# Kernel optimization log

Hardware: AMD Instinct MI355X
Metric: run time of the kernel (lower is better)

Reference implementation:

```python
import jax, jax.numpy as jnp
import numpy as np

N_NODES = 100000
N_EDGES = 1600000
D = 128
L = 3


def setup_inputs() -> dict:
    key = jax.random.key(0)
    ks = jax.random.split(key, 5)
    x = jax.random.normal(ks[0], (N_NODES, D), dtype=jnp.float32)
    # Xavier-ish scale for stability through 3 layers
    scale = 1.0 / np.sqrt(D)
    W_self = jax.random.normal(ks[1], (L, D, D), dtype=jnp.float32) * scale
    W_neigh = jax.random.normal(ks[2], (L, D, D), dtype=jnp.float32) * scale
    bias = jnp.zeros((L, D), dtype=jnp.float32)
    src = jax.random.randint(ks[3], (N_EDGES,), 0, N_NODES)
    dst = jax.random.randint(ks[4], (N_EDGES,), 0, N_NODES)
    return {"x": x, "W_self": W_self, "W_neigh": W_neigh, "bias": bias,
            "src": src, "dst": dst}


def reference(x, W_self, W_neigh, bias, src, dst):
    """HomoSAGEEncoder forward (inference mode, dropout = identity).

    Each layer: DGL SAGEConv('mean'):
        h_neigh[v] = mean_{u in in-neighbors(v)} h[u]   (0 if no neighbors)
        h = h @ W_self + h_neigh @ W_neigh + bias
    followed by ReLU.
    """
    N = x.shape[0]
    n_layers = W_self.shape[0]
    # in-degree per destination node (shared across layers)
    deg = jax.ops.segment_sum(jnp.ones_like(dst, dtype=x.dtype), dst,
                              num_segments=N)
    inv_deg = (1.0 / jnp.maximum(deg, 1.0))[:, None]  # [N,1]

    h = x
    for l in range(n_layers):
        msg = h[src]  # [E,D] gather
        h_neigh = jax.ops.segment_sum(msg, dst, num_segments=N) * inv_deg
        h = h @ W_self[l] + h_neigh @ W_neigh[l] + bias[l]
        h = jax.nn.relu(h)
        # dropout is identity at inference; skipped
    return h
```

## Files before the change

### kernel.cpp

```cpp
#include <hip/hip_runtime.h>

typedef __attribute__((ext_vector_type(8))) short short8;
typedef __attribute__((ext_vector_type(4))) float f32x4;

static constexpr int NN = 100000;
static constexpr int NE = 1600000;
static constexpr int DD = 128;
static constexpr int SCAN_CHUNK = 1024;
static constexpr int NB = (NN + SCAN_CHUNK - 1) / SCAN_CHUNK;

static constexpr int OFF_DEG  = 0;
static constexpr int OFF_OFFS = NN;
static constexpr int OFF_CUR  = 2*NN + 2;
static constexpr int OFF_WT   = 2*NN + 4;
static constexpr int OFF_PART = 3*NN + 8;
static constexpr int OFF_INV  = 3*NN + 512;
static constexpr int OFF_SS   = 4*NN + 512;
static constexpr int OFF_HB   = 4*NN + 512 + NE;
static constexpr int OFF_HNB  = OFF_HB + NN*64;
static constexpr int ZERO_N   = 3*NN + 264;

__device__ inline ushort f2b(float f) {
  uint u = __builtin_bit_cast(uint, f);
  uint r = (u + 0x7fffu + ((u >> 16) & 1u)) >> 16;
  return (ushort)r;
}
__device__ inline float b2f(ushort b) {
  uint u = ((uint)b) << 16;
  return __builtin_bit_cast(float, u);
}

__global__ void k_zero(int* ws) {
  int i = blockIdx.x * blockDim.x + threadIdx.x;
  if (i < ZERO_N) ws[i] = 0;
}

__global__ void k_x2b(const float* __restrict__ x, ushort* __restrict__ hb) {
  int i = blockIdx.x * blockDim.x + threadIdx.x;
  if (i < NN * (DD / 2)) {
    float2 v = *(const float2*)(x + (size_t)i * 2);
    uint p = (uint)f2b(v.x) | ((uint)f2b(v.y) << 16);
    *(uint*)(hb + (size_t)i * 2) = p;
  }
}

__global__ void k_hist(const int* __restrict__ dst, int* __restrict__ deg) {
  int e = blockIdx.x * blockDim.x + threadIdx.x;
  if (e < NE) atomicAdd(&deg[dst[e]], 1);
}

__global__ void k_scan1(const int* __restrict__ deg, int* __restrict__ offs,
                        int* __restrict__ partials) {
  __shared__ int sc[256];
  int b = blockIdx.x, t = threadIdx.x;
  int base = b * SCAN_CHUNK + t * 4;
  int d0 = (base + 0 < NN) ? deg[base + 0] : 0;
  int d1 = (base + 1 < NN) ? deg[base + 1] : 0;
  int d2 = (base + 2 < NN) ? deg[base + 2] : 0;
  int d3 = (base + 3 < NN) ? deg[base + 3] : 0;
  int s = d0 + d1 + d2 + d3;
  sc[t] = s;
  __syncthreads();
  for (int off = 1; off < 256; off <<= 1) {
    int v = (t >= off) ? sc[t - off] : 0;
    __syncthreads();
    sc[t] += v;
    __syncthreads();
  }
  int ebase = sc[t] - s;
  if (base + 0 < NN) offs[base + 0] = ebase;
  if (base + 1 < NN) offs[base + 1] = ebase + d0;
  if (base + 2 < NN) offs[base + 2] = ebase + d0 + d1;
  if (base + 3 < NN) offs[base + 3] = ebase + d0 + d1 + d2;
  if (t == 255) partials[b] = sc[255];
}

__global__ void k_scan2(int* __restrict__ partials) {
  __shared__ int sc[128];
  int t = threadIdx.x;
  int p = (t < NB) ? partials[t] : 0;
  sc[t] = p;
  __syncthreads();
  for (int off = 1; off < 128; off <<= 1) {
    int v = (t >= off) ? sc[t - off] : 0;
    __syncthreads();
    sc[t] += v;
    __syncthreads();
  }
  if (t < NB) partials[t] = sc[t] - p;
}

__global__ void k_scan3(const int* __restrict__ deg, int* __restrict__ offs,
                        const int* __restrict__ partials, float* __restrict__ inv_deg) {
  int i = blockIdx.x * blockDim.x + threadIdx.x;
  if (i < NN) {
    offs[i] += partials[i / SCAN_CHUNK];
    int d = deg[i];
    inv_deg[i] = 1.0f / (float)(d > 1 ? d : 1);
  }
  if (i == 0) offs[NN] = NE;
}

__global__ void k_scatter(const int* __restrict__ src, const int* __restrict__ dst,
                          const int* __restrict__ offs, int* __restrict__ cursor,
                          int* __restrict__ ss) {
  int e = blockIdx.x * blockDim.x + threadIdx.x;
  if (e < NE) {
    int d = dst[e];
    int pos = offs[d] + atomicAdd(&cursor[d], 1);
    ss[pos] = src[e];
  }
}

__global__ void k_wt(const float* __restrict__ Ws, const float* __restrict__ Wn,
                     ushort* __restrict__ Wt) {
  int i = blockIdx.x * blockDim.x + threadIdx.x;
  if (i < 3 * 128 * 256) {
    int l = i >> 15;
    int rem = i & 32767;
    int col = rem >> 8;
    int k = rem & 255;
    float v = (k < 128) ? Ws[((size_t)l * 128 + k) * 128 + col]
                        : Wn[((size_t)l * 128 + (k - 128)) * 128 + col];
    Wt[i] = f2b(v);
  }
}

__global__ void k_agg_bf(const ushort* __restrict__ h, const int* __restrict__ offs,
                         const int* __restrict__ ss, const float* __restrict__ inv_deg,
                         ushort* __restrict__ hN) {
  int wid  = (blockIdx.x * blockDim.x + threadIdx.x) >> 6;
  int lane = threadIdx.x & 63;
  int nw   = (gridDim.x * blockDim.x) >> 6;
  for (int v = wid; v < NN; v += nw) {
    int beg = offs[v], end = offs[v + 1];
    float sx0 = 0.f, sy0 = 0.f, sx1 = 0.f, sy1 = 0.f;
    float sx2 = 0.f, sy2 = 0.f, sx3 = 0.f, sy3 = 0.f;
    float sx4 = 0.f, sy4 = 0.f, sx5 = 0.f, sy5 = 0.f;
    float sx6 = 0.f, sy6 = 0.f, sx7 = 0.f, sy7 = 0.f;
    int e = beg;
    for (; e + 7 < end; e += 8) {
      uint u0 = *(const uint*)(h + (size_t)ss[e + 0] * DD + lane * 2);
      uint u1 = *(const uint*)(h + (size_t)ss[e + 1] * DD + lane * 2);
      uint u2 = *(const uint*)(h + (size_t)ss[e + 2] * DD + lane * 2);
      uint u3 = *(const uint*)(h + (size_t)ss[e + 3] * DD + lane * 2);
      uint u4 = *(const uint*)(h + (size_t)ss[e + 4] * DD + lane * 2);
      uint u5 = *(const uint*)(h + (size_t)ss[e + 5] * DD + lane * 2);
      uint u6 = *(const uint*)(h + (size_t)ss[e + 6] * DD + lane * 2);
      uint u7 = *(const uint*)(h + (size_t)ss[e + 7] * DD + lane * 2);
      sx0 += b2f((ushort)u0); sy0 += b2f((ushort)(u0 >> 16));
      sx1 += b2f((ushort)u1); sy1 += b2f((ushort)(u1 >> 16));
      sx2 += b2f((ushort)u2); sy2 += b2f((ushort)(u2 >> 16));
      sx3 += b2f((ushort)u3); sy3 += b2f((ushort)(u3 >> 16));
      sx4 += b2f((ushort)u4); sy4 += b2f((ushort)(u4 >> 16));
      sx5 += b2f((ushort)u5); sy5 += b2f((ushort)(u5 >> 16));
      sx6 += b2f((ushort)u6); sy6 += b2f((ushort)(u6 >> 16));
      sx7 += b2f((ushort)u7); sy7 += b2f((ushort)(u7 >> 16));
    }
    for (; e < end; ++e) {
      uint u0 = *(const uint*)(h + (size_t)ss[e] * DD + lane * 2);
      sx0 += b2f((ushort)u0); sy0 += b2f((ushort)(u0 >> 16));
    }
    float w = inv_deg[v];
    float fx = ((sx0 + sx1) + (sx2 + sx3)) + ((sx4 + sx5) + (sx6 + sx7));
    float fy = ((sy0 + sy1) + (sy2 + sy3)) + ((sy4 + sy5) + (sy6 + sy7));
    fx *= w; fy *= w;
    uint p = (uint)f2b(fx) | ((uint)f2b(fy) << 16);
    *(uint*)(hN + (size_t)v * DD + lane * 2) = p;
  }
}

__global__ __launch_bounds__(256) void k_gemm_mfma(
    const ushort* __restrict__ hA, const ushort* __restrict__ hNb,
    const ushort* __restrict__ Wt, const float* __restrict__ bias,
    ushort* __restrict__ hOutB, float* __restrict__ outF, int writeF) {
  int w = threadIdx.x >> 6;
  int lane = threadIdx.x & 63;
  int row0 = blockIdx.x * 128 + w * 32;
  int r = lane & 15;
  int kg = lane >> 4;

  f32x4 acc[2][8];
#pragma unroll
  for (int mt = 0; mt < 2; ++mt)
#pragma unroll
    for (int nt = 0; nt < 8; ++nt) acc[mt][nt] = (f32x4)0.f;

  int ra0 = row0 + r;       if (ra0 >= NN) ra0 = NN - 1;
  int ra1 = row0 + 16 + r;  if (ra1 >= NN) ra1 = NN - 1;

#pragma unroll
  for (int kt = 0; kt < 8; ++kt) {
    const ushort* hs = (kt < 4) ? hA : hNb;
    int kk = (kt & 3) * 32 + kg * 8;
    short8 a0 = *(const short8*)(hs + (size_t)ra0 * DD + kk);
    short8 a1 = *(const short8*)(hs + (size_t)ra1 * DD + kk);
    int kw = kt * 32 + kg * 8;
#pragma unroll
    for (int nt = 0; nt < 8; ++nt) {
      short8 b = *(const short8*)(Wt + (size_t)(nt * 16 + r) * 256 + kw);
      acc[0][nt] = __builtin_amdgcn_mfma_f32_16x16x32_bf16(a0, b, acc[0][nt], 0, 0, 0);
      acc[1][nt] = __builtin_amdgcn_mfma_f32_16x16x32_bf16(a1, b, acc[1][nt], 0, 0, 0);
    }
  }

  float bv[8];
#pragma unroll
  for (int nt = 0; nt < 8; ++nt) bv[nt] = bias[nt * 16 + r];

  int kg4 = kg * 4;
#pragma unroll
  for (int mt = 0; mt < 2; ++mt) {
#pragma unroll
    for (int j = 0; j < 4; ++j) {
      int row = row0 + mt * 16 + kg4 + j;
      if (row < NN) {
#pragma unroll
        for (int nt = 0; nt < 8; ++nt) {
          float val = fmaxf(acc[mt][nt][j] + bv[nt], 0.f);
          hOutB[(size_t)row * DD + nt * 16 + r] = f2b(val);
          if (writeF) outF[(size_t)row * DD + nt * 16 + r] = val;
        }
      }
    }
  }
}

extern "C" void kernel_launch(void* const* d_in, const int* in_sizes, int n_in,
                              void* d_out, int out_size, void* d_ws, size_t ws_size,
                              hipStream_t stream) {
  const float* x    = (const float*)d_in[0];
  const float* Ws   = (const float*)d_in[1];
  const float* Wn   = (const float*)d_in[2];
  const float* bias = (const float*)d_in[3];
  const int*   src  = (const int*)d_in[4];
  const int*   dst  = (const int*)d_in[5];
  float* out = (float*)d_out;

  int* ws      = (int*)d_ws;
  int* deg     = ws + OFF_DEG;
  int* offs    = ws + OFF_OFFS;
  int* cur     = ws + OFF_CUR;
  ushort* Wt   = (ushort*)(ws + OFF_WT);
  int* part    = ws + OFF_PART;
  float* inv   = (float*)(ws + OFF_INV);
  int* ssorted = ws + OFF_SS;
  ushort* hB   = (ushort*)(ws + OFF_HB);
  ushort* hNb  = (ushort*)(ws + OFF_HNB);

  k_zero<<<(ZERO_N + 255) / 256, 256, 0, stream>>>(ws);
  k_x2b<<<(NN * (DD / 2) + 255) / 256, 256, 0, stream>>>(x, hB);
  k_hist<<<(NE + 255) / 256, 256, 0, stream>>>(dst, deg);
  k_scan1<<<NB, 256, 0, stream>>>(deg, offs, part);
  k_scan2<<<1, 128, 0, stream>>>(part);
  k_scan3<<<(NN + 255) / 256, 256, 0, stream>>>(deg, offs, part, inv);
  k_scatter<<<(NE + 255) / 256, 256, 0, stream>>>(src, dst, offs, cur, ssorted);
  k_wt<<<(3 * 128 * 256 + 255) / 256, 256, 0, stream>>>(Ws, Wn, Wt);

  for (int l = 0; l < 3; ++l) {
    k_agg_bf<<<2048, 256, 0, stream>>>(hB, offs, ssorted, inv, hNb);
    k_gemm_mfma<<<(NN + 127) / 128, 256, 0, stream>>>(
        hB, hNb, Wt + (size_t)l * 256 * 128, bias + l * DD, hB, out, l == 2 ? 1 : 0);
  }
}
```

Before: 620.4 us.

## Bucket edges by destination range before histogram/scatter; half-wave per node aggregation

```diff
diff --git a/kernel.cpp b/kernel.cpp
--- a/kernel.cpp
+++ b/kernel.cpp
@@ -8,17 +8,21 @@
 static constexpr int DD = 128;
 static constexpr int SCAN_CHUNK = 1024;
 static constexpr int NB = (NN + SCAN_CHUNK - 1) / SCAN_CHUNK;
+static constexpr int NBUCK = 98;
+static constexpr int CAP = 18432;
 
 static constexpr int OFF_DEG  = 0;
 static constexpr int OFF_OFFS = NN;
 static constexpr int OFF_CUR  = 2*NN + 2;
-static constexpr int OFF_WT   = 2*NN + 4;
-static constexpr int OFF_PART = 3*NN + 8;
-static constexpr int OFF_INV  = 3*NN + 512;
-static constexpr int OFF_SS   = 4*NN + 512;
-static constexpr int OFF_HB   = 4*NN + 512 + NE;
+static constexpr int OFF_GCUR = 3*NN + 8;
+static constexpr int OFF_PART = 3*NN + 136;
+static constexpr int OFF_INV  = 3*NN + 264;
+static constexpr int OFF_WT   = 4*NN + 264;
+static constexpr int OFF_SS   = 4*NN + 49416;
+static constexpr int OFF_HB   = 4*NN + 49416 + NE;
 static constexpr int OFF_HNB  = OFF_HB + NN*64;
-static constexpr int ZERO_N   = 3*NN + 264;
+static constexpr int ZERO_BASE = OFF_CUR;
+static constexpr int ZERO_N    = NN + 134;
 
 __device__ inline ushort f2b(float f) {
   uint u = __builtin_bit_cast(uint, f);
@@ -30,9 +34,9 @@
   return __builtin_bit_cast(float, u);
 }
 
-__global__ void k_zero(int* ws) {
+__global__ void k_zero(int* p) {
   int i = blockIdx.x * blockDim.x + threadIdx.x;
-  if (i < ZERO_N) ws[i] = 0;
+  if (i < ZERO_N) p[i] = 0;
 }
 
 __global__ void k_x2b(const float* __restrict__ x, ushort* __restrict__ hb) {
@@ -44,9 +48,70 @@
   }
 }
 
-__global__ void k_hist(const int* __restrict__ dst, int* __restrict__ deg) {
-  int e = blockIdx.x * blockDim.x + threadIdx.x;
-  if (e < NE) atomicAdd(&deg[dst[e]], 1);
+__global__ void k_wt(const float* __restrict__ Ws, const float* __restrict__ Wn,
+                     ushort* __restrict__ Wt) {
+  int i = blockIdx.x * blockDim.x + threadIdx.x;
+  if (i < 3 * 128 * 256) {
+    int l = i >> 15;
+    int rem = i & 32767;
+    int col = rem >> 8;
+    int k = rem & 255;
+    float v = (k < 128) ? Ws[((size_t)l * 128 + k) * 128 + col]
+                        : Wn[((size_t)l * 128 + (k - 128)) * 128 + col];
+    Wt[i] = f2b(v);
+  }
+}
+
+__global__ __launch_bounds__(256) void k_bucket(const int* __restrict__ src,
+                                                const int* __restrict__ dst,
+                                                int* __restrict__ gcur,
+                                                int2* __restrict__ ebuf) {
+  __shared__ int cnt[NBUCK], base[NBUCK];
+  int t = threadIdx.x;
+  int b0 = blockIdx.x * 4096;
+  if (t < NBUCK) cnt[t] = 0;
+  __syncthreads();
+  int dv[16], pv[16];
+#pragma unroll
+  for (int j = 0; j < 16; ++j) {
+    int idx = b0 + j * 256 + t;
+    if (idx < NE) {
+      int d = dst[idx];
+      dv[j] = d;
+      pv[j] = atomicAdd(&cnt[d >> 10], 1);
+    } else dv[j] = -1;
+  }
+  __syncthreads();
+  if (t < NBUCK) base[t] = atomicAdd(&gcur[t], cnt[t]);
+  __syncthreads();
+#pragma unroll
+  for (int j = 0; j < 16; ++j) {
+    if (dv[j] >= 0) {
+      int idx = b0 + j * 256 + t;
+      int b = dv[j] >> 10;
+      int2 pr; pr.x = src[idx]; pr.y = dv[j];
+      ebuf[(size_t)b * CAP + base[b] + pv[j]] = pr;
+    }
+  }
+}
+
+__global__ __launch_bounds__(256) void k_hist2(const int2* __restrict__ ebuf,
+                                               const int* __restrict__ gcur,
+                                               int* __restrict__ deg) {
+  __shared__ int hist[1024];
+  int b = blockIdx.x, t = threadIdx.x;
+#pragma unroll
+  for (int j = 0; j < 4; ++j) hist[t + j * 256] = 0;
+  __syncthreads();
+  int n = gcur[b];
+  const int2* eb = ebuf + (size_t)b * CAP;
+  for (int i = t; i < n; i += 256) atomicAdd(&hist[eb[i].y & 1023], 1);
+  __syncthreads();
+#pragma unroll
+  for (int j = 0; j < 4; ++j) {
+    int node = b * 1024 + t + j * 256;
+    if (node < NN) deg[node] = hist[t + j * 256];
+  }
 }
 
 __global__ void k_scan1(const int* __restrict__ deg, int* __restrict__ offs,
@@ -101,72 +166,65 @@
   if (i == 0) offs[NN] = NE;
 }
 
-__global__ void k_scatter(const int* __restrict__ src, const int* __restrict__ dst,
-                          const int* __restrict__ offs, int* __restrict__ cursor,
-                          int* __restrict__ ss) {
-  int e = blockIdx.x * blockDim.x + threadIdx.x;
-  if (e < NE) {
-    int d = dst[e];
-    int pos = offs[d] + atomicAdd(&cursor[d], 1);
-    ss[pos] = src[e];
-  }
-}
-
-__global__ void k_wt(const float* __restrict__ Ws, const float* __restrict__ Wn,
-                     ushort* __restrict__ Wt) {
-  int i = blockIdx.x * blockDim.x + threadIdx.x;
-  if (i < 3 * 128 * 256) {
-    int l = i >> 15;
-    int rem = i & 32767;
-    int col = rem >> 8;
-    int k = rem & 255;
-    float v = (k < 128) ? Ws[((size_t)l * 128 + k) * 128 + col]
-                        : Wn[((size_t)l * 128 + (k - 128)) * 128 + col];
-    Wt[i] = f2b(v);
-  }
-}
-
-__global__ void k_agg_bf(const ushort* __restrict__ h, const int* __restrict__ offs,
-                         const int* __restrict__ ss, const float* __restrict__ inv_deg,
-                         ushort* __restrict__ hN) {
-  int wid  = (blockIdx.x * blockDim.x + threadIdx.x) >> 6;
+__global__ __launch_bounds__(256) void k_scatter2(const int2* __restrict__ ebuf,
+                                                  const int* __restrict__ gcur,
+                                                  const int* __restrict__ offs,
+                                                  int* __restrict__ cur,
+                                                  int* __restrict__ ss) {
+  int b = blockIdx.x >> 2, q = blockIdx.x & 3, t = threadIdx.x;
+  int n = gcur[b];
+  int lo = (int)((long long)n * q / 4), hi = (int)((long long)n * (q + 1) / 4);
+  const int2* eb = ebuf + (size_t)b * CAP;
+  for (int i = lo + t; i < hi; i += 256) {
+    int2 e = eb[i];
+    int pos = offs[e.y] + atomicAdd(&cur[e.y], 1);
+    ss[pos] = e.x;
+  }
+}
+
+__global__ void k_agg2(const ushort* __restrict__ h, const int* __restrict__ offs,
+                       const int* __restrict__ ss, const float* __restrict__ inv_deg,
+                       ushort* __restrict__ hN) {
+  int gid = blockIdx.x * blockDim.x + threadIdx.x;
+  int wid = gid >> 6;
   int lane = threadIdx.x & 63;
-  int nw   = (gridDim.x * blockDim.x) >> 6;
-  for (int v = wid; v < NN; v += nw) {
+  int half = lane >> 5, l32 = lane & 31;
+  int nw = (gridDim.x * blockDim.x) >> 6;
+  for (int vp = wid; vp < NN / 2; vp += nw) {
+    int v = vp * 2 + half;
     int beg = offs[v], end = offs[v + 1];
-    float sx0 = 0.f, sy0 = 0.f, sx1 = 0.f, sy1 = 0.f;
-    float sx2 = 0.f, sy2 = 0.f, sx3 = 0.f, sy3 = 0.f;
-    float sx4 = 0.f, sy4 = 0.f, sx5 = 0.f, sy5 = 0.f;
-    float sx6 = 0.f, sy6 = 0.f, sx7 = 0.f, sy7 = 0.f;
+    float a0=0,a1=0,a2=0,a3=0, b0=0,b1=0,b2=0,b3=0;
+    float c0=0,c1=0,c2=0,c3=0, d0=0,d1=0,d2=0,d3=0;
     int e = beg;
-    for (; e + 7 < end; e += 8) {
-      uint u0 = *(const uint*)(h + (size_t)ss[e + 0] * DD + lane * 2);
-      uint u1 = *(const uint*)(h + (size_t)ss[e + 1] * DD + lane * 2);
-      uint u2 = *(const uint*)(h + (size_t)ss[e + 2] * DD + lane * 2);
-      uint u3 = *(const uint*)(h + (size_t)ss[e + 3] * DD + lane * 2);
-      uint u4 = *(const uint*)(h + (size_t)ss[e + 4] * DD + lane * 2);
-      uint u5 = *(const uint*)(h + (size_t)ss[e + 5] * DD + lane * 2);
-      uint u6 = *(const uint*)(h + (size_t)ss[e + 6] * DD + lane * 2);
-      uint u7 = *(const uint*)(h + (size_t)ss[e + 7] * DD + lane * 2);
-      sx0 += b2f((ushort)u0); sy0 += b2f((ushort)(u0 >> 16));
-      sx1 += b2f((ushort)u1); sy1 += b2f((ushort)(u1 >> 16));
-      sx2 += b2f((ushort)u2); sy2 += b2f((ushort)(u2 >> 16));
-      sx3 += b2f((ushort)u3); sy3 += b2f((ushort)(u3 >> 16));
-      sx4 += b2f((ushort)u4); sy4 += b2f((ushort)(u4 >> 16));
-      sx5 += b2f((ushort)u5); sy5 += b2f((ushort)(u5 >> 16));
-      sx6 += b2f((ushort)u6); sy6 += b2f((ushort)(u6 >> 16));
-      sx7 += b2f((ushort)u7); sy7 += b2f((ushort)(u7 >> 16));
+    for (; e + 3 < end; e += 4) {
+      uint2 u0 = *(const uint2*)(h + (size_t)ss[e + 0] * DD + l32 * 4);
+      uint2 u1 = *(const uint2*)(h + (size_t)ss[e + 1] * DD + l32 * 4);
+      uint2 u2 = *(const uint2*)(h + (size_t)ss[e + 2] * DD + l32 * 4);
+      uint2 u3 = *(const uint2*)(h + (size_t)ss[e + 3] * DD + l32 * 4);
+      a0 += b2f((ushort)u0.x); a1 += b2f((ushort)(u0.x >> 16));
+      a2 += b2f((ushort)u0.y); a3 += b2f((ushort)(u0.y >> 16));
+      b0 += b2f((ushort)u1.x); b1 += b2f((ushort)(u1.x >> 16));
+      b2 += b2f((ushort)u1.y); b3 += b2f((ushort)(u1.y >> 16));
+      c0 += b2f((ushort)u2.x); c1 += b2f((ushort)(u2.x >> 16));
+      c2 += b2f((ushort)u2.y); c3 += b2f((ushort)(u2.y >> 16));
+      d0 += b2f((ushort)u3.x); d1 += b2f((ushort)(u3.x >> 16));
+      d2 += b2f((ushort)u3.y); d3 += b2f((ushort)(u3.y >> 16));
     }
     for (; e < end; ++e) {
-      uint u0 = *(const uint*)(h + (size_t)ss[e] * DD + lane * 2);
-      sx0 += b2f((ushort)u0); sy0 += b2f((ushort)(u0 >> 16));
+      uint2 u0 = *(const uint2*)(h + (size_t)ss[e] * DD + l32 * 4);
+      a0 += b2f((ushort)u0.x); a1 += b2f((ushort)(u0.x >> 16));
+      a2 += b2f((ushort)u0.y); a3 += b2f((ushort)(u0.y >> 16));
     }
     float w = inv_deg[v];
-    float fx = ((sx0 + sx1) + (sx2 + sx3)) + ((sx4 + sx5) + (sx6 + sx7));
-    float fy = ((sy0 + sy1) + (sy2 + sy3)) + ((sy4 + sy5) + (sy6 + sy7));
-    fx *= w; fy *= w;
-    uint p = (uint)f2b(fx) | ((uint)f2b(fy) << 16);
-    *(uint*)(hN + (size_t)v * DD + lane * 2) = p;
+    float f0 = (a0 + b0) + (c0 + d0);
+    float f1 = (a1 + b1) + (c1 + d1);
+    float f2 = (a2 + b2) + (c2 + d2);
+    float f3 = (a3 + b3) + (c3 + d3);
+    f0 *= w; f1 *= w; f2 *= w; f3 *= w;
+    uint2 p;
+    p.x = (uint)f2b(f0) | ((uint)f2b(f1) << 16);
+    p.y = (uint)f2b(f2) | ((uint)f2b(f3) << 16);
+    *(uint2*)(hN + (size_t)v * DD + l32 * 4) = p;
   }
 }
 
@@ -241,24 +299,27 @@
   int* deg     = ws + OFF_DEG;
   int* offs    = ws + OFF_OFFS;
   int* cur     = ws + OFF_CUR;
-  ushort* Wt   = (ushort*)(ws + OFF_WT);
+  int* gcur    = ws + OFF_GCUR;
   int* part    = ws + OFF_PART;
   float* inv   = (float*)(ws + OFF_INV);
+  ushort* Wt   = (ushort*)(ws + OFF_WT);
   int* ssorted = ws + OFF_SS;
   ushort* hB   = (ushort*)(ws + OFF_HB);
   ushort* hNb  = (ushort*)(ws + OFF_HNB);
-
-  k_zero<<<(ZERO_N + 255) / 256, 256, 0, stream>>>(ws);
+  int2* ebuf   = (int2*)(ws + OFF_HNB);
+
+  k_zero<<<(ZERO_N + 255) / 256, 256, 0, stream>>>(ws + ZERO_BASE);
   k_x2b<<<(NN * (DD / 2) + 255) / 256, 256, 0, stream>>>(x, hB);
-  k_hist<<<(NE + 255) / 256, 256, 0, stream>>>(dst, deg);
+  k_wt<<<(3 * 128 * 256 + 255) / 256, 256, 0, stream>>>(Ws, Wn, Wt);
+  k_bucket<<<(NE + 4095) / 4096, 256, 0, stream>>>(src, dst, gcur, ebuf);
+  k_hist2<<<NBUCK, 256, 0, stream>>>(ebuf, gcur, deg);
   k_scan1<<<NB, 256, 0, stream>>>(deg, offs, part);
   k_scan2<<<1, 128, 0, stream>>>(part);
   k_scan3<<<(NN + 255) / 256, 256, 0, stream>>>(deg, offs, part, inv);
-  k_scatter<<<(NE + 255) / 256, 256, 0, stream>>>(src, dst, offs, cur, ssorted);
-  k_wt<<<(3 * 128 * 256 + 255) / 256, 256, 0, stream>>>(Ws, Wn, Wt);
+  k_scatter2<<<NBUCK * 4, 256, 0, stream>>>(ebuf, gcur, offs, cur, ssorted);
 
   for (int l = 0; l < 3; ++l) {
-    k_agg_bf<<<2048, 256, 0, stream>>>(hB, offs, ssorted, inv, hNb);
+    k_agg2<<<2048, 256, 0, stream>>>(hB, offs, ssorted, inv, hNb);
     k_gemm_mfma<<<(NN + 127) / 128, 256, 0, stream>>>(
         hB, hNb, Wt + (size_t)l * 256 * 128, bias + l * DD, hB, out, l == 2 ? 1 : 0);
   }
```

Measured after the change: 609.8 us. Within noise of the previous version (-1.7%).
